# Optimization experiments

Measured on AMD Instinct MI355X. Metric: run time of the kernel, lower is better.

## Reference

```python
import jax, jax.numpy as jnp
import numpy as np

NEG = -1e30  # finite stand-in for -inf so logaddexp grads stay clean
ADVERSARY_WEIGHT = 0.5


def _bfctc(logits, targets, act_lens, tgt_lens):
    """Blank-free CTC negative log-likelihood, size_average=True (mean over batch).

    logits: (T, B, C) unnormalized activations (log_softmax applied internally,
            as in warp-ctc style bindings).
    targets: (B, U) int label ids (padding beyond tgt_lens is ignored).
    Alignment lattice: at each frame stay on the same label or advance one
    label (no blank state):
        alpha[t, u] = logaddexp(alpha[t-1, u], alpha[t-1, u-1]) + logp[t, y_u]
    Loss per utterance = -alpha[act_len-1, tgt_len-1].
    """
    T, B, C = logits.shape
    U = targets.shape[1]
    logprobs = jax.nn.log_softmax(logits, axis=-1)  # (T,B,C)
    idx = jnp.broadcast_to(targets[None], (T, B, U))
    lp = jnp.take_along_axis(logprobs, idx, axis=2)  # (T,B,U) logp of each target label per frame

    alpha0 = lp[0] + jnp.where(jnp.arange(U) == 0, 0.0, NEG)[None, :]  # (B,U)

    def step(alpha, inp):
        lp_t, t = inp
        shifted = jnp.concatenate(
            [jnp.full((B, 1), NEG, alpha.dtype), alpha[:, :-1]], axis=1)
        new = jnp.logaddexp(alpha, shifted) + lp_t
        # freeze alpha once past this utterance's frame length
        alpha = jnp.where((t < act_lens)[:, None], new, alpha)
        return alpha, None

    alpha, _ = jax.lax.scan(step, alpha0, (lp[1:], jnp.arange(1, T)))
    loss_b = -jnp.take_along_axis(alpha, (tgt_lens - 1)[:, None], axis=1)[:, 0]
    return jnp.mean(loss_b)  # size_average=True


def reference(x, W, b, ctc_target_p1, ctc_target_p2, ctc_acts_lens,
              ctc_target_lens_p1, ctc_target_lens_p2):
    # output_layer projection then (B,T,C) -> (T,B,C), float32 cast
    logits = (x @ W + b)
    acts = jnp.transpose(logits, (1, 0, 2)).astype(jnp.float32)
    l1 = _bfctc(acts, ctc_target_p1, ctc_acts_lens, ctc_target_lens_p1)
    l2 = _bfctc(acts, ctc_target_p2, ctc_acts_lens, ctc_target_lens_p2)
    return (l1 - ADVERSARY_WEIGHT * l2, l1, l2)


def setup_inputs() -> dict:
    B, T, U, D, C = 16, 2000, 400, 512, 4096
    key = jax.random.key(0)
    k = jax.random.split(key, 8)
    x = jax.random.normal(k[0], (B, T, D), dtype=jnp.float32)
    W = jax.random.normal(k[1], (D, C), dtype=jnp.float32) * 0.02
    b = jnp.zeros((C,), dtype=jnp.float32)
    tgt1 = jax.random.randint(k[2], (B, U), 0, C)
    tgt2 = jax.random.randint(k[3], (B, U), 0, C)
    # frame lengths in [T//2, T) so every target (U<=400) has a valid alignment
    act_lens = jax.random.randint(k[4], (B,), T // 2, T)
    tlen1 = jax.random.randint(k[5], (B,), 1, U + 1)
    tlen2 = jax.random.randint(k[6], (B,), 1, U + 1)
    return {
        "x": x, "W": W, "b": b,
        "ctc_target_p1": tgt1, "ctc_target_p2": tgt2,
        "ctc_acts_lens": act_lens,
        "ctc_target_lens_p1": tlen1, "ctc_target_lens_p2": tlen2,
    }
```

## Files before the change

### kernel.cpp

```cpp
#include <hip/hip_runtime.h>
#include <hip/hip_bf16.h>
#include <stdint.h>

constexpr int B_ = 16;
constexpr int T_ = 2000;
constexpr int U_ = 400;
constexpr int D_ = 512;
constexpr int C_ = 4096;
constexpr int U2P_ = 896;
constexpr float LN2F = 0.6931471805599453f;

typedef __attribute__((ext_vector_type(8))) short bf16x8;
typedef __attribute__((ext_vector_type(4))) float f32x4;
typedef __attribute__((ext_vector_type(8))) unsigned short us8;

__device__ __forceinline__ ushort f2bf(float f) {
  uint32_t u = __builtin_bit_cast(uint32_t, f);
  uint32_t r = (u + 0x7fffu + ((u >> 16) & 1u)) >> 16;
  return (ushort)r;
}

__device__ __forceinline__ float bf2f(ushort h) {
  return __builtin_bit_cast(float, (uint32_t)h << 16);
}

__device__ __forceinline__ void async_copy16(const void* gptr, void* ldsptr) {
  __builtin_amdgcn_global_load_lds(
      (const __attribute__((address_space(1))) uint32_t*)gptr,
      (__attribute__((address_space(3))) uint32_t*)ldsptr,
      16, 0, 0);
}

__global__ void cvt_bf16_k(const float* __restrict__ in, ushort* __restrict__ out, int n4) {
  int i = blockIdx.x * blockDim.x + threadIdx.x;
  int stride = gridDim.x * blockDim.x;
  for (; i < n4; i += stride) {
    float4 v = ((const float4*)in)[i];
    ushort4 o;
    o.x = f2bf(v.x); o.y = f2bf(v.y); o.z = f2bf(v.z); o.w = f2bf(v.w);
    ((ushort4*)out)[i] = o;
  }
}

__global__ void transposeW_k(const float* __restrict__ W, ushort* __restrict__ Wt) {
  __shared__ float tile[32][33];
  int c0 = blockIdx.x * 32, d0 = blockIdx.y * 32;
  int tx = threadIdx.x, ty = threadIdx.y;
  #pragma unroll
  for (int i = 0; i < 4; ++i) {
    int r = ty + i * 8;
    tile[r][tx] = W[(size_t)(d0 + r) * C_ + c0 + tx];
  }
  __syncthreads();
  #pragma unroll
  for (int i = 0; i < 4; ++i) {
    int r = ty + i * 8;
    Wt[(size_t)(c0 + r) * D_ + d0 + tx] = f2bf(tile[tx][r]);
  }
}

__global__ void gatherW_k(const ushort* __restrict__ Wt, const float* __restrict__ bias,
                          const int* __restrict__ t1, const int* __restrict__ t2,
                          ushort* __restrict__ Wgt, float* __restrict__ biasg) {
  int u2 = blockIdx.x;
  int b = blockIdx.y;
  int tid = threadIdx.x;
  int set = u2 >= 448;
  int us = u2 - (set ? 448 : 0);
  int c = (us < U_) ? (set ? t2 : t1)[b * U_ + us] : -1;
  ushort4 v; v.x = 0; v.y = 0; v.z = 0; v.w = 0;
  if (c >= 0) v = *(const ushort4*)(Wt + (size_t)c * D_ + tid * 4);
  *(ushort4*)(Wgt + ((size_t)b * U2P_ + u2) * D_ + tid * 4) = v;
  if (tid == 0) biasg[b * U2P_ + u2] = (c >= 0) ? bias[c] : 0.f;
}

#define BM 128
#define BN 128
#define BKK 64

__global__ __launch_bounds__(256) void gemm_lse_k(
    const ushort* __restrict__ A, const ushort* __restrict__ Bt,
    const float* __restrict__ bias, float* __restrict__ lsesum) {
  constexpr int K = D_;
  __shared__ __align__(16) ushort As[BM * BKK];
  __shared__ __align__(16) ushort Bs[BN * BKK];
  const int tid = threadIdx.x;
  const int wid = tid >> 6, lane = tid & 63;
  const int wr = wid >> 1, wc = wid & 1;
  const int bn = blockIdx.x, bm = blockIdx.y;
  const ushort* Ab = A + (size_t)bm * BM * K;
  const ushort* Bb = Bt + (size_t)bn * BN * K;
  f32x4 acc[4][4];
  #pragma unroll
  for (int m = 0; m < 4; ++m)
    #pragma unroll
    for (int n = 0; n < 4; ++n) {
      f32x4 z = {0.f, 0.f, 0.f, 0.f};
      acc[m][n] = z;
    }

  for (int kt = 0; kt < K; kt += BKK) {
    __syncthreads();
    #pragma unroll
    for (int i = 0; i < 4; ++i) {
      int o = (i * 4 + wid) * 64 + lane;
      int row = o >> 3;
      int gc = (o & 7) ^ (row & 7);
      async_copy16(Ab + (size_t)row * K + kt + gc * 8, &As[(size_t)(i * 4 + wid) * 64 * 8]);
      async_copy16(Bb + (size_t)row * K + kt + gc * 8, &Bs[(size_t)(i * 4 + wid) * 64 * 8]);
    }
    asm volatile("s_waitcnt vmcnt(0)" ::: "memory");
    __syncthreads();
    #pragma unroll
    for (int ks = 0; ks < 2; ++ks) {
      bf16x8 af[4], bfr[4];
      #pragma unroll
      for (int m = 0; m < 4; ++m) {
        int row = wr * 64 + m * 16 + (lane & 15);
        int c16 = (ks * 4 + (lane >> 4)) ^ (row & 7);
        af[m] = *(const bf16x8*)((const char*)As + row * 128 + c16 * 16);
      }
      #pragma unroll
      for (int n = 0; n < 4; ++n) {
        int row = wc * 64 + n * 16 + (lane & 15);
        int c16 = (ks * 4 + (lane >> 4)) ^ (row & 7);
        bfr[n] = *(const bf16x8*)((const char*)Bs + row * 128 + c16 * 16);
      }
      #pragma unroll
      for (int m = 0; m < 4; ++m)
        #pragma unroll
        for (int n = 0; n < 4; ++n)
          acc[m][n] = __builtin_amdgcn_mfma_f32_16x16x32_bf16(af[m], bfr[n], acc[m][n], 0, 0, 0);
    }
  }
  float bv[4];
  #pragma unroll
  for (int n = 0; n < 4; ++n)
    bv[n] = bias[bn * BN + wc * 64 + n * 16 + (lane & 15)];
  #pragma unroll
  for (int m = 0; m < 4; ++m) {
    #pragma unroll
    for (int r = 0; r < 4; ++r) {
      float s = 0.f;
      #pragma unroll
      for (int n = 0; n < 4; ++n) s += __expf(acc[m][n][r] + bv[n]);
      s += __shfl_xor(s, 1);
      s += __shfl_xor(s, 2);
      s += __shfl_xor(s, 4);
      s += __shfl_xor(s, 8);
      if ((lane & 15) == 0) {
        int grow = bm * BM + wr * 64 + m * 16 + (lane >> 4) * 4 + r;
        atomicAdd(&lsesum[grow], s);
      }
    }
  }
}

__global__ __launch_bounds__(256) void gemm_lp_k(
    const ushort* __restrict__ xb, const ushort* __restrict__ Wgt,
    const float* __restrict__ biasg, ushort* __restrict__ cbuf) {
  constexpr int K = D_;
  __shared__ __align__(16) ushort As[BM * BKK];
  __shared__ __align__(16) ushort Bs[BN * BKK];
  const int tid = threadIdx.x;
  const int wid = tid >> 6, lane = tid & 63;
  const int wr = wid >> 1, wc = wid & 1;
  const int bn = blockIdx.x, bm = blockIdx.y, b = blockIdx.z;
  const ushort* Ab = xb + (size_t)b * T_ * K + (size_t)bm * BM * K;
  const ushort* Bb = Wgt + (size_t)b * U2P_ * K + (size_t)bn * BN * K;
  f32x4 acc[4][4];
  #pragma unroll
  for (int m = 0; m < 4; ++m)
    #pragma unroll
    for (int n = 0; n < 4; ++n) {
      f32x4 z = {0.f, 0.f, 0.f, 0.f};
      acc[m][n] = z;
    }

  for (int kt = 0; kt < K; kt += BKK) {
    __syncthreads();
    #pragma unroll
    for (int i = 0; i < 4; ++i) {
      int o = (i * 4 + wid) * 64 + lane;
      int row = o >> 3;
      int gc = (o & 7) ^ (row & 7);
      if (bm * BM + row < T_)
        async_copy16(Ab + (size_t)row * K + kt + gc * 8, &As[(size_t)(i * 4 + wid) * 64 * 8]);
      async_copy16(Bb + (size_t)row * K + kt + gc * 8, &Bs[(size_t)(i * 4 + wid) * 64 * 8]);
    }
    asm volatile("s_waitcnt vmcnt(0)" ::: "memory");
    __syncthreads();
    #pragma unroll
    for (int ks = 0; ks < 2; ++ks) {
      bf16x8 af[4], bfr[4];
      #pragma unroll
      for (int m = 0; m < 4; ++m) {
        int row = wr * 64 + m * 16 + (lane & 15);
        int c16 = (ks * 4 + (lane >> 4)) ^ (row & 7);
        af[m] = *(const bf16x8*)((const char*)As + row * 128 + c16 * 16);
      }
      #pragma unroll
      for (int n = 0; n < 4; ++n) {
        int row = wc * 64 + n * 16 + (lane & 15);
        int c16 = (ks * 4 + (lane >> 4)) ^ (row & 7);
        bfr[n] = *(const bf16x8*)((const char*)Bs + row * 128 + c16 * 16);
      }
      #pragma unroll
      for (int m = 0; m < 4; ++m)
        #pragma unroll
        for (int n = 0; n < 4; ++n)
          acc[m][n] = __builtin_amdgcn_mfma_f32_16x16x32_bf16(af[m], bfr[n], acc[m][n], 0, 0, 0);
    }
  }
  float bv[4];
  #pragma unroll
  for (int n = 0; n < 4; ++n)
    bv[n] = biasg[b * U2P_ + bn * BN + wc * 64 + n * 16 + (lane & 15)];
  #pragma unroll
  for (int m = 0; m < 4; ++m) {
    #pragma unroll
    for (int r = 0; r < 4; ++r) {
      int t = bm * BM + wr * 64 + m * 16 + (lane >> 4) * 4 + r;
      if (t < T_) {
        #pragma unroll
        for (int n = 0; n < 4; ++n) {
          int u2 = bn * BN + wc * 64 + n * 16 + (lane & 15);
          int set = u2 >= 448;
          int us = u2 - (set ? 448 : 0);
          float val = (us < U_) ? __expf(acc[m][n][r] + bv[n]) : 0.f;
          cbuf[((size_t)(b * 2 + set) * T_ + t) * 512 + us] = f2bf(val);
        }
      }
    }
  }
}

__global__ void lse_reduce_k(const float* __restrict__ lsesum, const int* __restrict__ act_lens,
                             float* __restrict__ S) {
  int b = blockIdx.x;
  int al = act_lens[b];
  float s = 0.f;
  for (int t = threadIdx.x; t < al; t += blockDim.x)
    s += logf(lsesum[b * T_ + t]);
  #pragma unroll
  for (int off = 32; off >= 1; off >>= 1) s += __shfl_xor(s, off);
  __shared__ float wsum[4];
  int w = threadIdx.x >> 6, lane = threadIdx.x & 63;
  if (lane == 0) wsum[w] = s;
  __syncthreads();
  if (threadIdx.x == 0) S[b] = wsum[0] + wsum[1] + wsum[2] + wsum[3];
}

__global__ __launch_bounds__(64) void bfctc_scan_k(
    const ushort* __restrict__ cbuf, const int* __restrict__ act_lens,
    const int* __restrict__ tl1, const int* __restrict__ tl2,
    float* __restrict__ rawloss) {
  int bi = blockIdx.x;
  int b = bi >> 1, set = bi & 1;
  int lane = threadIdx.x;
  int al = act_lens[b];
  int tl = (set ? tl2 : tl1)[b];
  const char* base = (const char*)cbuf + (size_t)bi * T_ * 1024 + lane * 16;

  float alpha[8];
  int E = 0;
  float bscale;

  {
    us8 c0 = *(const us8*)(base);
    float iv0 = bf2f(c0[0]);
    #pragma unroll
    for (int r = 0; r < 8; ++r) alpha[r] = 0.f;
    if (lane == 0) alpha[0] = iv0;
    bscale = (lane >= 50) ? 0.f : 1.0f;
  }

  auto step1 = [&](us8 c8) {
    int pi = __builtin_amdgcn_update_dpp(
        0, __builtin_bit_cast(int, alpha[7]), 0x138 , 0xf, 0xf, true);
    float prev = __builtin_bit_cast(float, pi) * bscale;
    float c[8];
    #pragma unroll
    for (int r = 0; r < 8; ++r) c[r] = bf2f(c8[r]);
    #pragma unroll
    for (int r = 7; r >= 1; --r)
      alpha[r] = (alpha[r] + alpha[r - 1]) * c[r];
    alpha[0] = (alpha[0] + prev) * c[0];
  };

  auto rescale = [&]() {
    float m01 = fmaxf(alpha[0], alpha[1]);
    float m23 = fmaxf(alpha[2], alpha[3]);
    float m45 = fmaxf(alpha[4], alpha[5]);
    float m67 = fmaxf(alpha[6], alpha[7]);
    float m = fmaxf(fmaxf(m01, m23), fmaxf(m45, m67));
    int mb = __builtin_bit_cast(int, m);
    bool dead = (mb == 0);
    int ei = ((mb >> 23) & 255) - 127;
    float s = __builtin_bit_cast(float, (127 - ei) << 23);
    #pragma unroll
    for (int r = 0; r < 8; ++r) alpha[r] *= s;
    if (!dead) E += ei;
    int pe = __builtin_amdgcn_update_dpp(0, E, 0x138, 0xf, 0xf, true);
    if (dead) E = pe;
    int dE = pe - E;
    dE = dE < -126 ? -126 : (dE > 126 ? 126 : dE);
    bscale = __builtin_bit_cast(float, (127 + dE) << 23);
    if (lane >= 50) bscale = 0.f;
  };

  us8 B0[8], B1[8], B2[8], B3[8];
  auto load0 = [&](int blk) {
    const char* p = base + (size_t)(1 + 8 * blk) * 1024;
    #pragma unroll
    for (int i = 0; i < 8; ++i) B0[i] = *(const us8*)(p + i * 1024);
  };
  auto load1 = [&](int blk) {
    const char* p = base + (size_t)(1 + 8 * blk) * 1024;
    #pragma unroll
    for (int i = 0; i < 8; ++i) B1[i] = *(const us8*)(p + i * 1024);
  };
  auto load2 = [&](int blk) {
    const char* p = base + (size_t)(1 + 8 * blk) * 1024;
    #pragma unroll
    for (int i = 0; i < 8; ++i) B2[i] = *(const us8*)(p + i * 1024);
  };
  auto load3 = [&](int blk) {
    const char* p = base + (size_t)(1 + 8 * blk) * 1024;
    #pragma unroll
    for (int i = 0; i < 8; ++i) B3[i] = *(const us8*)(p + i * 1024);
  };
  auto comp0 = [&]() {
    #pragma unroll
    for (int i = 0; i < 8; ++i) step1(B0[i]);
  };
  auto comp1 = [&]() {
    #pragma unroll
    for (int i = 0; i < 8; ++i) step1(B1[i]);
  };
  auto comp2 = [&]() {
    #pragma unroll
    for (int i = 0; i < 8; ++i) step1(B2[i]);
  };
  auto comp3 = [&]() {
    #pragma unroll
    for (int i = 0; i < 8; ++i) step1(B3[i]);
  };

  int S = al - 1;
  int nb = S >> 3;
  load0(0); load1(1); load2(2); load3(3);
  int j = 0;
  while (j + 4 <= nb) {
    comp0(); rescale(); load0(j + 4);
    comp1(); rescale(); load1(j + 5);
    comp2(); rescale(); load2(j + 6);
    comp3(); rescale(); load3(j + 7);
    j += 4;
  }
  if (j < nb)     { comp0(); rescale(); }
  if (j + 1 < nb) { comp1(); rescale(); }
  if (j + 2 < nb) { comp2(); rescale(); }
  for (int t = 1 + 8 * nb; t <= S; ++t) {
    us8 c = *(const us8*)(base + (size_t)t * 1024);
    step1(c);
  }

  int ui = tl - 1, lt = ui >> 3, rt = ui & 7;
  float v = alpha[0];
  #pragma unroll
  for (int r = 1; r < 8; ++r) v = (rt == r) ? alpha[r] : v;
  float tot = (__builtin_amdgcn_logf(v) + (float)E) * LN2F;
  tot = __shfl(tot, lt);
  if (lane == 0) rawloss[bi] = tot;
}

__global__ void combine_k(const float* __restrict__ S, const float* __restrict__ raw,
                          float* __restrict__ out) {
  int lane = threadIdx.x;
  float d1 = 0.f, d2 = 0.f;
  if (lane < 16) {
    d1 = S[lane] - raw[lane * 2 + 0];
    d2 = S[lane] - raw[lane * 2 + 1];
  }
  #pragma unroll
  for (int off = 8; off >= 1; off >>= 1) {
    d1 += __shfl_xor(d1, off);
    d2 += __shfl_xor(d2, off);
  }
  if (lane == 0) {
    float l1 = d1 * (1.f / 16.f), l2 = d2 * (1.f / 16.f);
    out[0] = l1 - 0.5f * l2;
    out[1] = l1;
    out[2] = l2;
  }
}

extern "C" void kernel_launch(void* const* d_in, const int* in_sizes, int n_in,
                              void* d_out, int out_size, void* d_ws, size_t ws_size,
                              hipStream_t stream) {
  const float* x    = (const float*)d_in[0];
  const float* W    = (const float*)d_in[1];
  const float* bias = (const float*)d_in[2];
  const int* t1  = (const int*)d_in[3];
  const int* t2  = (const int*)d_in[4];
  const int* al  = (const int*)d_in[5];
  const int* tl1 = (const int*)d_in[6];
  const int* tl2 = (const int*)d_in[7];
  float* out = (float*)d_out;

  char* ws = (char*)d_ws;
  size_t off = 0;
  auto alloc = [&](size_t bytes) -> char* {
    char* p = ws + off;
    off += (bytes + 255) & ~(size_t)255;
    return p;
  };
  ushort* xb     = (ushort*)alloc((size_t)B_ * T_ * D_ * 2);
  ushort* Wt     = (ushort*)alloc((size_t)C_ * D_ * 2);
  ushort* Wgt    = (ushort*)alloc((size_t)B_ * U2P_ * D_ * 2);
  float*  biasg  = (float*)alloc((size_t)B_ * U2P_ * 4);
  float*  lsesum = (float*)alloc((size_t)B_ * T_ * 4);
  ushort* cbuf   = (ushort*)alloc((size_t)2 * B_ * T_ * 512 * 2);
  alloc(65536);
  float*  Sb     = (float*)alloc(B_ * 4);
  float*  rawl   = (float*)alloc(2 * B_ * 4);
  (void)ws_size; (void)in_sizes; (void)n_in; (void)out_size;

  (void)hipMemsetAsync(lsesum, 0, (size_t)B_ * T_ * 4, stream);

  cvt_bf16_k<<<2048, 256, 0, stream>>>(x, xb, B_ * T_ * D_ / 4);
  transposeW_k<<<dim3(C_ / 32, D_ / 32), dim3(32, 8), 0, stream>>>(W, Wt);
  gatherW_k<<<dim3(U2P_, B_), 128, 0, stream>>>(Wt, bias, t1, t2, Wgt, biasg);

  gemm_lse_k<<<dim3(C_ / BN, (B_ * T_) / BM), 256, 0, stream>>>(xb, Wt, bias, lsesum);
  gemm_lp_k<<<dim3(U2P_ / BN, (T_ + BM - 1) / BM, B_), 256, 0, stream>>>(xb, Wgt, biasg, cbuf);

  lse_reduce_k<<<B_, 256, 0, stream>>>(lsesum, al, Sb);
  bfctc_scan_k<<<2 * B_, 64, 0, stream>>>(cbuf, al, tl1, tl2, rawl);
  combine_k<<<1, 64, 0, stream>>>(Sb, rawl, out);
}
```

Baseline: 527.5 us.

## Replace GEMM kernels with 256x256-tile, 8-wave, 4-stage pipelined MFMA kernel

The two separate 128x128 GEMM kernels (the log-sum-exp GEMM and the gathered-label GEMM) become one templated kernel. It uses 256x256 tiles, 512 threads and a 4-deep async global-to-LDS ring with a K-step of 32. Loads for step kt+3 are issued between the MFMA halves, guarded by explicit vmcnt waits, and s_setprio is raised around the MFMA bursts. The goal is to hide memory latency and get more reuse per LDS byte. In exchange, the padded label dimension grows to 1024, the row guard on A loads is dropped (it reads past T into neighbouring rows or buffers), and LDS use per block rises to 128KB.

```diff
diff --git a/kernel.cpp b/kernel.cpp
--- a/kernel.cpp
+++ b/kernel.cpp
@@ -7,7 +7,7 @@
 constexpr int U_ = 400;
 constexpr int D_ = 512;
 constexpr int C_ = 4096;
-constexpr int U2P_ = 896;
+constexpr int U2P_ = 1024;
 constexpr float LN2F = 0.6931471805599453f;
 
 typedef __attribute__((ext_vector_type(8))) short bf16x8;
@@ -65,8 +65,8 @@
   int u2 = blockIdx.x;
   int b = blockIdx.y;
   int tid = threadIdx.x;
-  int set = u2 >= 448;
-  int us = u2 - (set ? 448 : 0);
+  int set = u2 >= 512;
+  int us = u2 - (set ? 512 : 0);
   int c = (us < U_) ? (set ? t2 : t1)[b * U_ + us] : -1;
   ushort4 v; v.x = 0; v.y = 0; v.z = 0; v.w = 0;
   if (c >= 0) v = *(const ushort4*)(Wt + (size_t)c * D_ + tid * 4);
@@ -74,161 +74,154 @@
   if (tid == 0) biasg[b * U2P_ + u2] = (c >= 0) ? bias[c] : 0.f;
 }
 
-#define BM 128
-#define BN 128
-#define BKK 64
-
-__global__ __launch_bounds__(256) void gemm_lse_k(
+template <bool IS_LP>
+__global__ __launch_bounds__(512, 2) void gemm8_k(
     const ushort* __restrict__ A, const ushort* __restrict__ Bt,
-    const float* __restrict__ bias, float* __restrict__ lsesum) {
+    const float* __restrict__ biasp, float* __restrict__ lsesum,
+    ushort* __restrict__ cbuf) {
   constexpr int K = D_;
-  __shared__ __align__(16) ushort As[BM * BKK];
-  __shared__ __align__(16) ushort Bs[BN * BKK];
+  constexpr int NKT = K / 32;
+  __shared__ __align__(16) ushort As[4][8192];
+  __shared__ __align__(16) ushort Bs[4][8192];
   const int tid = threadIdx.x;
   const int wid = tid >> 6, lane = tid & 63;
-  const int wr = wid >> 1, wc = wid & 1;
-  const int bn = blockIdx.x, bm = blockIdx.y;
-  const ushort* Ab = A + (size_t)bm * BM * K;
-  const ushort* Bb = Bt + (size_t)bn * BN * K;
-  f32x4 acc[4][4];
-  #pragma unroll
-  for (int m = 0; m < 4; ++m)
-    #pragma unroll
-    for (int n = 0; n < 4; ++n) {
+  const int wr = wid >> 2, wc = wid & 3;
+  const int h = lane >> 4, lr = lane & 15;
+  const int bn = blockIdx.x, bm = blockIdx.y, bz = blockIdx.z;
+
+  const ushort* Ab = A + ((size_t)(IS_LP ? bz * T_ : 0) + (size_t)bm * 256) * K;
+  const ushort* Bb = Bt + ((size_t)(IS_LP ? bz * U2P_ : 0) + (size_t)bn * 256) * K;
+
+  auto stageA = [&](int buf, int kt, int j) {
+    int o = (j * 8 + wid) * 64 + lane;
+    int row = o >> 2;
+    int g = ((o & 3) - (row >> 1)) & 3;
+    async_copy16(Ab + (size_t)row * K + kt * 32 + g * 8,
+                 &As[buf][(size_t)(j * 8 + wid) * 512]);
+  };
+  auto stageB = [&](int buf, int kt, int j) {
+    int o = (j * 8 + wid) * 64 + lane;
+    int row = o >> 2;
+    int g = ((o & 3) - (row >> 1)) & 3;
+    async_copy16(Bb + (size_t)row * K + kt * 32 + g * 8,
+                 &Bs[buf][(size_t)(j * 8 + wid) * 512]);
+  };
+
+  f32x4 acc[8][4];
+  #pragma unroll
+  for (int mi = 0; mi < 8; ++mi)
+    #pragma unroll
+    for (int ni = 0; ni < 4; ++ni) {
       f32x4 z = {0.f, 0.f, 0.f, 0.f};
-      acc[m][n] = z;
-    }
-
-  for (int kt = 0; kt < K; kt += BKK) {
-    __syncthreads();
-    #pragma unroll
-    for (int i = 0; i < 4; ++i) {
-      int o = (i * 4 + wid) * 64 + lane;
-      int row = o >> 3;
-      int gc = (o & 7) ^ (row & 7);
-      async_copy16(Ab + (size_t)row * K + kt + gc * 8, &As[(size_t)(i * 4 + wid) * 64 * 8]);
-      async_copy16(Bb + (size_t)row * K + kt + gc * 8, &Bs[(size_t)(i * 4 + wid) * 64 * 8]);
-    }
-    asm volatile("s_waitcnt vmcnt(0)" ::: "memory");
-    __syncthreads();
-    #pragma unroll
-    for (int ks = 0; ks < 2; ++ks) {
-      bf16x8 af[4], bfr[4];
-      #pragma unroll
-      for (int m = 0; m < 4; ++m) {
-        int row = wr * 64 + m * 16 + (lane & 15);
-        int c16 = (ks * 4 + (lane >> 4)) ^ (row & 7);
-        af[m] = *(const bf16x8*)((const char*)As + row * 128 + c16 * 16);
-      }
-      #pragma unroll
-      for (int n = 0; n < 4; ++n) {
-        int row = wc * 64 + n * 16 + (lane & 15);
-        int c16 = (ks * 4 + (lane >> 4)) ^ (row & 7);
-        bfr[n] = *(const bf16x8*)((const char*)Bs + row * 128 + c16 * 16);
-      }
-      #pragma unroll
-      for (int m = 0; m < 4; ++m)
+      acc[mi][ni] = z;
+    }
+
+  for (int kt = 0; kt < 3; ++kt) {
+    stageA(kt, kt, 0); stageA(kt, kt, 1);
+    stageB(kt, kt, 0); stageB(kt, kt, 1);
+  }
+
+  for (int kt = 0; kt < NKT; ++kt) {
+    const int buf = kt & 3;
+    if (kt <= NKT - 3)      asm volatile("s_waitcnt vmcnt(8)" ::: "memory");
+    else if (kt == NKT - 2) asm volatile("s_waitcnt vmcnt(4)" ::: "memory");
+    else                    asm volatile("s_waitcnt vmcnt(0)" ::: "memory");
+    __builtin_amdgcn_s_barrier();
+    __builtin_amdgcn_sched_barrier(0);
+
+    bf16x8 bfr[4];
+    #pragma unroll
+    for (int ni = 0; ni < 4; ++ni) {
+      int row = wc * 64 + ni * 16 + lr;
+      int c16 = (h + (row >> 1)) & 3;
+      bfr[ni] = *(const bf16x8*)(&Bs[buf][row * 32 + c16 * 8]);
+    }
+    {
+      bf16x8 af[4];
+      #pragma unroll
+      for (int mi = 0; mi < 4; ++mi) {
+        int row = wr * 128 + mi * 16 + lr;
+        int c16 = (h + (row >> 1)) & 3;
+        af[mi] = *(const bf16x8*)(&As[buf][row * 32 + c16 * 8]);
+      }
+      if (kt + 3 < NKT) {
+        stageA((kt + 3) & 3, kt + 3, 0);
+        stageA((kt + 3) & 3, kt + 3, 1);
+      }
+      __builtin_amdgcn_s_barrier();
+      __builtin_amdgcn_s_setprio(1);
+      #pragma unroll
+      for (int mi = 0; mi < 4; ++mi)
         #pragma unroll
-        for (int n = 0; n < 4; ++n)
-          acc[m][n] = __builtin_amdgcn_mfma_f32_16x16x32_bf16(af[m], bfr[n], acc[m][n], 0, 0, 0);
-    }
-  }
-  float bv[4];
-  #pragma unroll
-  for (int n = 0; n < 4; ++n)
-    bv[n] = bias[bn * BN + wc * 64 + n * 16 + (lane & 15)];
-  #pragma unroll
-  for (int m = 0; m < 4; ++m) {
-    #pragma unroll
-    for (int r = 0; r < 4; ++r) {
-      float s = 0.f;
-      #pragma unroll
-      for (int n = 0; n < 4; ++n) s += __expf(acc[m][n][r] + bv[n]);
-      s += __shfl_xor(s, 1);
-      s += __shfl_xor(s, 2);
-      s += __shfl_xor(s, 4);
-      s += __shfl_xor(s, 8);
-      if ((lane & 15) == 0) {
-        int grow = bm * BM + wr * 64 + m * 16 + (lane >> 4) * 4 + r;
-        atomicAdd(&lsesum[grow], s);
-      }
-    }
-  }
-}
-
-__global__ __launch_bounds__(256) void gemm_lp_k(
-    const ushort* __restrict__ xb, const ushort* __restrict__ Wgt,
-    const float* __restrict__ biasg, ushort* __restrict__ cbuf) {
-  constexpr int K = D_;
-  __shared__ __align__(16) ushort As[BM * BKK];
-  __shared__ __align__(16) ushort Bs[BN * BKK];
-  const int tid = threadIdx.x;
-  const int wid = tid >> 6, lane = tid & 63;
-  const int wr = wid >> 1, wc = wid & 1;
-  const int bn = blockIdx.x, bm = blockIdx.y, b = blockIdx.z;
-  const ushort* Ab = xb + (size_t)b * T_ * K + (size_t)bm * BM * K;
-  const ushort* Bb = Wgt + (size_t)b * U2P_ * K + (size_t)bn * BN * K;
-  f32x4 acc[4][4];
-  #pragma unroll
-  for (int m = 0; m < 4; ++m)
-    #pragma unroll
-    for (int n = 0; n < 4; ++n) {
-      f32x4 z = {0.f, 0.f, 0.f, 0.f};
-      acc[m][n] = z;
-    }
-
-  for (int kt = 0; kt < K; kt += BKK) {
-    __syncthreads();
-    #pragma unroll
-    for (int i = 0; i < 4; ++i) {
-      int o = (i * 4 + wid) * 64 + lane;
-      int row = o >> 3;
-      int gc = (o & 7) ^ (row & 7);
-      if (bm * BM + row < T_)
-        async_copy16(Ab + (size_t)row * K + kt + gc * 8, &As[(size_t)(i * 4 + wid) * 64 * 8]);
-      async_copy16(Bb + (size_t)row * K + kt + gc * 8, &Bs[(size_t)(i * 4 + wid) * 64 * 8]);
-    }
-    asm volatile("s_waitcnt vmcnt(0)" ::: "memory");
-    __syncthreads();
-    #pragma unroll
-    for (int ks = 0; ks < 2; ++ks) {
-      bf16x8 af[4], bfr[4];
-      #pragma unroll
-      for (int m = 0; m < 4; ++m) {
-        int row = wr * 64 + m * 16 + (lane & 15);
-        int c16 = (ks * 4 + (lane >> 4)) ^ (row & 7);
-        af[m] = *(const bf16x8*)((const char*)As + row * 128 + c16 * 16);
-      }
-      #pragma unroll
-      for (int n = 0; n < 4; ++n) {
-        int row = wc * 64 + n * 16 + (lane & 15);
-        int c16 = (ks * 4 + (lane >> 4)) ^ (row & 7);
-        bfr[n] = *(const bf16x8*)((const char*)Bs + row * 128 + c16 * 16);
-      }
-      #pragma unroll
-      for (int m = 0; m < 4; ++m)
+        for (int ni = 0; ni < 4; ++ni)
+          acc[mi][ni] = __builtin_amdgcn_mfma_f32_16x16x32_bf16(af[mi], bfr[ni], acc[mi][ni], 0, 0, 0);
+      __builtin_amdgcn_s_setprio(0);
+      __builtin_amdgcn_s_barrier();
+    }
+    {
+      bf16x8 af[4];
+      #pragma unroll
+      for (int mi = 0; mi < 4; ++mi) {
+        int row = wr * 128 + (mi + 4) * 16 + lr;
+        int c16 = (h + (row >> 1)) & 3;
+        af[mi] = *(const bf16x8*)(&As[buf][row * 32 + c16 * 8]);
+      }
+      if (kt + 3 < NKT) {
+        stageB((kt + 3) & 3, kt + 3, 0);
+        stageB((kt + 3) & 3, kt + 3, 1);
+      }
+      __builtin_amdgcn_s_barrier();
+      __builtin_amdgcn_s_setprio(1);
+      #pragma unroll
+      for (int mi = 0; mi < 4; ++mi)
         #pragma unroll
-        for (int n = 0; n < 4; ++n)
-          acc[m][n] = __builtin_amdgcn_mfma_f32_16x16x32_bf16(af[m], bfr[n], acc[m][n], 0, 0, 0);
-    }
-  }
-  float bv[4];
-  #pragma unroll
-  for (int n = 0; n < 4; ++n)
-    bv[n] = biasg[b * U2P_ + bn * BN + wc * 64 + n * 16 + (lane & 15)];
-  #pragma unroll
-  for (int m = 0; m < 4; ++m) {
-    #pragma unroll
-    for (int r = 0; r < 4; ++r) {
-      int t = bm * BM + wr * 64 + m * 16 + (lane >> 4) * 4 + r;
-      if (t < T_) {
+        for (int ni = 0; ni < 4; ++ni)
+          acc[mi + 4][ni] = __builtin_amdgcn_mfma_f32_16x16x32_bf16(af[mi], bfr[ni], acc[mi + 4][ni], 0, 0, 0);
+      __builtin_amdgcn_s_setprio(0);
+    }
+  }
+
+  if constexpr (!IS_LP) {
+    float bv[4];
+    #pragma unroll
+    for (int ni = 0; ni < 4; ++ni)
+      bv[ni] = biasp[bn * 256 + wc * 64 + ni * 16 + lr];
+    #pragma unroll
+    for (int mi = 0; mi < 8; ++mi) {
+      #pragma unroll
+      for (int r = 0; r < 4; ++r) {
+        float s = 0.f;
         #pragma unroll
-        for (int n = 0; n < 4; ++n) {
-          int u2 = bn * BN + wc * 64 + n * 16 + (lane & 15);
-          int set = u2 >= 448;
-          int us = u2 - (set ? 448 : 0);
-          float val = (us < U_) ? __expf(acc[m][n][r] + bv[n]) : 0.f;
-          cbuf[((size_t)(b * 2 + set) * T_ + t) * 512 + us] = f2bf(val);
+        for (int ni = 0; ni < 4; ++ni) s += __expf(acc[mi][ni][r] + bv[ni]);
+        s += __shfl_xor(s, 1);
+        s += __shfl_xor(s, 2);
+        s += __shfl_xor(s, 4);
+        s += __shfl_xor(s, 8);
+        if (lr == 0) {
+          int grow = bm * 256 + wr * 128 + mi * 16 + h * 4 + r;
+          atomicAdd(&lsesum[grow], s);
+        }
+      }
+    }
+  } else {
+    float bv[4];
+    #pragma unroll
+    for (int ni = 0; ni < 4; ++ni)
+      bv[ni] = biasp[bz * U2P_ + bn * 256 + wc * 64 + ni * 16 + lr];
+    #pragma unroll
+    for (int mi = 0; mi < 8; ++mi) {
+      #pragma unroll
+      for (int r = 0; r < 4; ++r) {
+        int t = bm * 256 + wr * 128 + mi * 16 + h * 4 + r;
+        if (t < T_) {
+          #pragma unroll
+          for (int ni = 0; ni < 4; ++ni) {
+            int u2 = bn * 256 + wc * 64 + ni * 16 + lr;
+            int set = u2 >> 9;
+            int us = u2 & 511;
+            float val = (us < U_) ? __expf(acc[mi][ni][r] + bv[ni]) : 0.f;
+            cbuf[((size_t)(bz * 2 + set) * T_ + t) * 512 + us] = f2bf(val);
+          }
         }
       }
     }
@@ -433,8 +426,10 @@
   transposeW_k<<<dim3(C_ / 32, D_ / 32), dim3(32, 8), 0, stream>>>(W, Wt);
   gatherW_k<<<dim3(U2P_, B_), 128, 0, stream>>>(Wt, bias, t1, t2, Wgt, biasg);
 
-  gemm_lse_k<<<dim3(C_ / BN, (B_ * T_) / BM), 256, 0, stream>>>(xb, Wt, bias, lsesum);
-  gemm_lp_k<<<dim3(U2P_ / BN, (T_ + BM - 1) / BM, B_), 256, 0, stream>>>(xb, Wgt, biasg, cbuf);
+  gemm8_k<false><<<dim3(C_ / 256, (B_ * T_) / 256, 1), 512, 0, stream>>>(
+      xb, Wt, bias, lsesum, nullptr);
+  gemm8_k<true><<<dim3(U2P_ / 256, 2048 / 256, B_), 512, 0, stream>>>(
+      xb, Wgt, biasg, nullptr, cbuf);
 
   lse_reduce_k<<<B_, 256, 0, stream>>>(lsesum, al, Sb);
   bfctc_scan_k<<<2 * B_, 64, 0, stream>>>(cbuf, al, tl1, tl2, rawl);
```

After: 478.5 us. -9.3%, faster.
